# Optimization experiments

Hardware: AMD Instinct MI355X
Metric: run time of the kernel (lower is better)

Reference implementation:

```python
import jax, jax.numpy as jnp
import numpy as np

B_SZ, N_IN, N_CTX, UNITS, RANK = 4096, 4096, 512, 4096, 256


def setup_inputs() -> dict:
    key = jax.random.key(0)
    ks = jax.random.split(key, 8)
    inputs = jax.random.normal(ks[0], (B_SZ, N_IN), dtype=jnp.float32)
    context = jax.random.normal(ks[1], (B_SZ, N_CTX), dtype=jnp.float32)
    # Orthogonal-ish init approximated by scaled normals (math-equivalent shapes)
    U = jax.random.normal(ks[2], (N_IN, RANK), dtype=jnp.float32) / np.sqrt(N_IN)
    S = jax.random.uniform(ks[3], (RANK,), dtype=jnp.float32, minval=0.5, maxval=1.5)
    V = jax.random.normal(ks[4], (UNITS, RANK), dtype=jnp.float32) / np.sqrt(UNITS)
    W = jax.random.normal(ks[5], (N_CTX, RANK), dtype=jnp.float32) / np.sqrt(N_CTX)
    B = jnp.zeros((RANK,), dtype=jnp.float32)
    bias = jnp.zeros((UNITS,), dtype=jnp.float32)
    return {"inputs": inputs, "context": context, "U": U, "S": S, "V": V, "W": W, "B": B, "bias": bias}


def reference(inputs, context, U, S, V, W, B, bias):
    # chi[b,r] = sigmoid(context @ W + B)
    chi = jax.nn.sigmoid(context @ W + B)                  # [B, R]
    # Original: kernel[b,n,m] = sum_r U[n,r]*S[r]*chi[b,r]*V[m,r];
    # out[b,m] = sum_n x[b,n]*kernel[b,n,m]. Algebraically equal to:
    t = (inputs @ U) * (S * chi)                           # [B, R]
    out = t @ V.T + bias                                   # first '+ self.bias'
    out = out + bias                                       # 'outputs += self.bias' (use_bias=True)
    return jax.nn.relu(out)
```

## Files before the change

kernel.cpp:

```cpp
#include <hip/hip_runtime.h>

#define B_SZ 4096
#define N_IN 4096
#define N_CTX 512
#define UNITS 4096
#define RANK 256
#define ZSPLIT 8

typedef __attribute__((ext_vector_type(8))) __bf16 bf16x8;
typedef __attribute__((ext_vector_type(4))) float f32x4;
typedef __attribute__((ext_vector_type(8))) unsigned short ushort8;
typedef __attribute__((ext_vector_type(4))) unsigned short ushort4v;

__device__ __forceinline__ unsigned short f2bf(float f) {
    unsigned int u = __float_as_uint(f);
    u += 0x7FFFu + ((u >> 16) & 1u);
    return (unsigned short)(u >> 16);
}
__device__ __forceinline__ float bf2f(unsigned short h) {
    return __uint_as_float(((unsigned int)h) << 16);
}
__device__ __forceinline__ void gload_lds16(const unsigned short* g, unsigned short* l) {
    __builtin_amdgcn_global_load_lds(
        (const __attribute__((address_space(1))) unsigned int*)g,
        (__attribute__((address_space(3))) unsigned int*)l, 16, 0, 0);
}
__device__ __forceinline__ bf16x8 ldfrag(const unsigned short* p) {
    ushort8 t = *(const ushort8*)p;
    return __builtin_bit_cast(bf16x8, t);
}

__global__ void prep(const float* __restrict__ U, const float* __restrict__ W,
                     const float* __restrict__ V,
                     unsigned short* __restrict__ UT, unsigned short* __restrict__ WT,
                     unsigned short* __restrict__ Vb) {
    __shared__ unsigned short t[64][66];
    int bid = blockIdx.x, tid = threadIdx.x;
    if (bid < 288) {
        const float* src; unsigned short* dst; int R, C, rb, cb;
        if (bid < 256) { src = U; dst = UT; R = N_IN; C = RANK; rb = (bid & 63) * 64; cb = (bid >> 6) * 64; }
        else { int b = bid - 256; src = W; dst = WT; R = N_CTX; C = RANK; rb = (b & 7) * 64; cb = (b >> 3) * 64; }
        int r = tid >> 4, c4 = (tid & 15) * 4;
        for (int i = 0; i < 4; i++) {
            float4 v = *(const float4*)(src + (size_t)(rb + r + i * 16) * C + cb + c4);
            t[r + i * 16][c4 + 0] = f2bf(v.x);
            t[r + i * 16][c4 + 1] = f2bf(v.y);
            t[r + i * 16][c4 + 2] = f2bf(v.z);
            t[r + i * 16][c4 + 3] = f2bf(v.w);
        }
        __syncthreads();
        int c = tid >> 3, r8 = (tid & 7) * 8;
        for (int j = 0; j < 2; j++) {
            int cc = c + j * 32;
            ushort8 o;
            for (int k = 0; k < 8; k++) o[k] = t[r8 + k][cc];
            *(ushort8*)(dst + (size_t)(cb + cc) * R + rb + r8) = o;
        }
    } else {
        size_t base = (size_t)(bid - 288) * 2048 + (size_t)tid * 8;
        float4 a = *(const float4*)(V + base);
        float4 b = *(const float4*)(V + base + 4);
        ushort8 o = { f2bf(a.x), f2bf(a.y), f2bf(a.z), f2bf(a.w),
                      f2bf(b.x), f2bf(b.y), f2bf(b.z), f2bf(b.w) };
        *(ushort8*)(Vb + base) = o;
    }
}


__launch_bounds__(256, 4)
__global__ void k1_chi(const float* __restrict__ ctx, const unsigned short* __restrict__ WT,
                       const float* __restrict__ S, const float* __restrict__ Bb,
                       unsigned short* __restrict__ Schi) {
    __shared__ unsigned short As[32 * 64];
    __shared__ unsigned short Bs[64 * 64];
    int tid = threadIdx.x, w = tid >> 6, lane = tid & 63;
    int ln15 = lane & 15, quad = lane >> 4;
    int wr = w >> 1, wc = w & 1;
    int tm = blockIdx.y * 32, tn = blockIdx.x * 64;
    f32x4 acc2[2] = {};
    int arow = tid >> 3, acs = tid & 7;
    const float* ag = ctx + (size_t)(tm + arow) * N_CTX + acs * 8;
    unsigned short* al = As + arow * 64 + (acs ^ (arow & 7)) * 8;
    int bl8 = lane >> 3, bcs = lane & 7;
    int bgc = (bcs ^ bl8) * 8;
    for (int kt = 0; kt < 8; kt++) {
        int k0 = kt * 64;
        for (int c = 0; c < 2; c++) {
            int row = w * 16 + c * 8 + bl8;
            gload_lds16(WT + (size_t)(tn + row) * N_CTX + k0 + bgc, Bs + row * 64 + bcs * 8);
        }
        {
            float4 v0 = *(const float4*)(ag + k0);
            float4 v1 = *(const float4*)(ag + k0 + 4);
            ushort8 a8 = { f2bf(v0.x), f2bf(v0.y), f2bf(v0.z), f2bf(v0.w),
                           f2bf(v1.x), f2bf(v1.y), f2bf(v1.z), f2bf(v1.w) };
            *(ushort8*)al = a8;
        }
        __syncthreads();
        for (int kh = 0; kh < 2; kh++) {
            int ch = kh * 4 + quad;
            bf16x8 af = ldfrag(As + (wr * 16 + ln15) * 64 + (ch ^ (ln15 & 7)) * 8);
            for (int j = 0; j < 2; j++) {
                int row = wc * 32 + j * 16 + ln15;
                bf16x8 bfr = ldfrag(Bs + row * 64 + (ch ^ (ln15 & 7)) * 8);
                acc2[j] = __builtin_amdgcn_mfma_f32_16x16x32_bf16(af, bfr, acc2[j], 0, 0, 0);
            }
        }
        __syncthreads();
    }
    for (int j = 0; j < 2; j++) {
        int col = tn + wc * 32 + j * 16 + ln15;
        float sv = S[col], bv = Bb[col];
        for (int r = 0; r < 4; r++) {
            int row = tm + wr * 16 + quad * 4 + r;
            float x = acc2[j][r] + bv;
            float chi = sv / (1.f + __expf(-x));
            Schi[(size_t)row * RANK + col] = f2bf(chi);
        }
    }
}

__launch_bounds__(256, 4)
__global__ void k2_t0(const float* __restrict__ X, const unsigned short* __restrict__ UT,
                      unsigned short* __restrict__ T0p) {
    __shared__ unsigned short As[64 * 64];
    __shared__ unsigned short Bs[128 * 64];
    int tid = threadIdx.x, w = tid >> 6, lane = tid & 63;
    int ln15 = lane & 15, quad = lane >> 4;
    int wr = w >> 1, wc = w & 1;
    int tm = blockIdx.y * 64, tn = blockIdx.x * 128;
    int kbase = blockIdx.z * (N_IN / ZSPLIT);
    f32x4 acc[2][4] = {};
    int arow = tid >> 2, acs0 = tid & 3;
    const float* ag = X + (size_t)(tm + arow) * N_IN + kbase;
    unsigned short* al0 = As + arow * 64 + ((acs0 + 0) ^ (arow & 7)) * 8;
    unsigned short* al1 = As + arow * 64 + ((acs0 + 4) ^ (arow & 7)) * 8;
    int bl8 = lane >> 3, bcs = lane & 7;
    int bgc = (bcs ^ bl8) * 8;
    for (int kt = 0; kt < (N_IN / ZSPLIT) / 64; kt++) {
        int k0 = kt * 64;
        for (int c = 0; c < 4; c++) {
            int row = w * 32 + c * 8 + bl8;
            gload_lds16(UT + (size_t)(tn + row) * N_IN + kbase + k0 + bgc, Bs + row * 64 + bcs * 8);
        }
        {
            float4 v0 = *(const float4*)(ag + k0 + acs0 * 8);
            float4 v1 = *(const float4*)(ag + k0 + acs0 * 8 + 4);
            float4 u0 = *(const float4*)(ag + k0 + (acs0 + 4) * 8);
            float4 u1 = *(const float4*)(ag + k0 + (acs0 + 4) * 8 + 4);
            ushort8 a8 = { f2bf(v0.x), f2bf(v0.y), f2bf(v0.z), f2bf(v0.w),
                           f2bf(v1.x), f2bf(v1.y), f2bf(v1.z), f2bf(v1.w) };
            ushort8 b8 = { f2bf(u0.x), f2bf(u0.y), f2bf(u0.z), f2bf(u0.w),
                           f2bf(u1.x), f2bf(u1.y), f2bf(u1.z), f2bf(u1.w) };
            *(ushort8*)al0 = a8;
            *(ushort8*)al1 = b8;
        }
        __syncthreads();
        for (int kh = 0; kh < 2; kh++) {
            int ch = kh * 4 + quad;
            int sw = (ch ^ (ln15 & 7)) * 8;
            bf16x8 af[2], bfr[4];
            for (int i = 0; i < 2; i++)
                af[i] = ldfrag(As + (wr * 32 + i * 16 + ln15) * 64 + sw);
            for (int j = 0; j < 4; j++)
                bfr[j] = ldfrag(Bs + (wc * 64 + j * 16 + ln15) * 64 + sw);
            for (int i = 0; i < 2; i++)
                for (int j = 0; j < 4; j++)
                    acc[i][j] = __builtin_amdgcn_mfma_f32_16x16x32_bf16(af[i], bfr[j], acc[i][j], 0, 0, 0);
        }
        __syncthreads();
    }
    unsigned short* P = T0p + (size_t)blockIdx.z * B_SZ * RANK;
    for (int i = 0; i < 2; i++)
        for (int j = 0; j < 4; j++) {
            int col = tn + wc * 64 + j * 16 + ln15;
            for (int r = 0; r < 4; r++) {
                int row = tm + wr * 32 + i * 16 + quad * 4 + r;
                P[(size_t)row * RANK + col] = f2bf(acc[i][j][r]);
            }
        }
}

__global__ void e_red(const unsigned short* __restrict__ T0p, const unsigned short* __restrict__ Schi,
                      unsigned short* __restrict__ T) {
    int i = blockIdx.x * 256 + threadIdx.x;
    const size_t stride = (size_t)B_SZ * RANK;
    float a[8] = {};
    for (int z = 0; z < ZSPLIT; z++) {
        ushort8 p = *(const ushort8*)(T0p + z * stride + (size_t)i * 8);
        for (int k = 0; k < 8; k++) a[k] += bf2f(p[k]);
    }
    ushort8 s = *(const ushort8*)(Schi + (size_t)i * 8);
    ushort8 o;
    for (int k = 0; k < 8; k++) o[k] = f2bf(a[k] * bf2f(s[k]));
    *(ushort8*)(T + (size_t)i * 8) = o;
}

__launch_bounds__(256, 4)
__global__ void k3_out(const unsigned short* __restrict__ T, const unsigned short* __restrict__ Vb,
                       const float* __restrict__ bias, float* __restrict__ out) {
    __shared__ unsigned short As[64 * 64];
    __shared__ unsigned short Bs[128 * 64];
    int tid = threadIdx.x, w = tid >> 6, lane = tid & 63;
    int ln15 = lane & 15, quad = lane >> 4;
    int wr = w >> 1, wc = w & 1;
    int tn = blockIdx.x * 128, tm = blockIdx.y * 64;
    f32x4 acc[2][4] = {};
    int bl8 = lane >> 3, bcs = lane & 7;
    int bgc = (bcs ^ bl8) * 8;
    for (int kt = 0; kt < RANK / 64; kt++) {
        int k0 = kt * 64;
        for (int c = 0; c < 2; c++) {
            int row = w * 16 + c * 8 + bl8;
            gload_lds16(T + (size_t)(tm + row) * RANK + k0 + bgc, As + row * 64 + bcs * 8);
        }
        for (int c = 0; c < 4; c++) {
            int row = w * 32 + c * 8 + bl8;
            gload_lds16(Vb + (size_t)(tn + row) * RANK + k0 + bgc, Bs + row * 64 + bcs * 8);
        }
        __syncthreads();
        for (int kh = 0; kh < 2; kh++) {
            int ch = kh * 4 + quad;
            int sw = (ch ^ (ln15 & 7)) * 8;
            bf16x8 af[2], bfr[4];
            for (int i = 0; i < 2; i++)
                af[i] = ldfrag(As + (wr * 32 + i * 16 + ln15) * 64 + sw);
            for (int j = 0; j < 4; j++)
                bfr[j] = ldfrag(Bs + (wc * 64 + j * 16 + ln15) * 64 + sw);
            for (int i = 0; i < 2; i++)
                for (int j = 0; j < 4; j++)
                    acc[i][j] = __builtin_amdgcn_mfma_f32_16x16x32_bf16(af[i], bfr[j], acc[i][j], 0, 0, 0);
        }
        __syncthreads();
    }
    for (int j = 0; j < 4; j++) {
        int col = tn + wc * 64 + j * 16 + ln15;
        float bv = 2.f * bias[col];
        for (int i = 0; i < 2; i++)
            for (int r = 0; r < 4; r++) {
                int row = tm + wr * 32 + i * 16 + quad * 4 + r;
                float v = acc[i][j][r] + bv;
                out[(size_t)row * UNITS + col] = fmaxf(v, 0.f);
            }
    }
}

extern "C" void kernel_launch(void* const* d_in, const int* in_sizes, int n_in,
                              void* d_out, int out_size, void* d_ws, size_t ws_size,
                              hipStream_t stream) {
    (void)in_sizes; (void)n_in; (void)out_size; (void)ws_size;
    const float* inputs  = (const float*)d_in[0];
    const float* context = (const float*)d_in[1];
    const float* U       = (const float*)d_in[2];
    const float* S       = (const float*)d_in[3];
    const float* V       = (const float*)d_in[4];
    const float* W       = (const float*)d_in[5];
    const float* Bb      = (const float*)d_in[6];
    const float* bias    = (const float*)d_in[7];
    float* out = (float*)d_out;

    char* ws = (char*)d_ws;
    size_t o = 0;
    unsigned short* UT   = (unsigned short*)(ws + o); o += (size_t)RANK * N_IN * 2;
    unsigned short* WT   = (unsigned short*)(ws + o); o += (size_t)RANK * N_CTX * 2;
    unsigned short* Vb   = (unsigned short*)(ws + o); o += (size_t)UNITS * RANK * 2;
    unsigned short* Schi = (unsigned short*)(ws + o); o += (size_t)B_SZ * RANK * 2;
    unsigned short* T    = (unsigned short*)(ws + o); o += (size_t)B_SZ * RANK * 2;
    unsigned short* T0p  = (unsigned short*)(ws + o); o += (size_t)ZSPLIT * B_SZ * RANK * 2;

    prep<<<800, 256, 0, stream>>>(U, W, V, UT, WT, Vb);
    k2_t0<<<dim3(RANK / 128, B_SZ / 64, ZSPLIT), 256, 0, stream>>>(inputs, UT, T0p);
    k1_chi<<<dim3(RANK / 64, B_SZ / 32), 256, 0, stream>>>(context, WT, S, Bb, Schi);
    e_red<<<(B_SZ * RANK) / (256 * 8), 256, 0, stream>>>(T0p, Schi, T);
    k3_out<<<dim3(UNITS / 128, B_SZ / 64), 256, 0, stream>>>(T, Vb, bias, out);
}
```

Before: 178.8 us.

## Replace LDS-staged GEMM tiles with per-wave direct global fragment loads

```diff
diff --git a/kernel.cpp b/kernel.cpp
--- a/kernel.cpp
+++ b/kernel.cpp
@@ -10,7 +10,6 @@
 typedef __attribute__((ext_vector_type(8))) __bf16 bf16x8;
 typedef __attribute__((ext_vector_type(4))) float f32x4;
 typedef __attribute__((ext_vector_type(8))) unsigned short ushort8;
-typedef __attribute__((ext_vector_type(4))) unsigned short ushort4v;
 
 __device__ __forceinline__ unsigned short f2bf(float f) {
     unsigned int u = __float_as_uint(f);
@@ -20,15 +19,16 @@
 __device__ __forceinline__ float bf2f(unsigned short h) {
     return __uint_as_float(((unsigned int)h) << 16);
 }
-__device__ __forceinline__ void gload_lds16(const unsigned short* g, unsigned short* l) {
-    __builtin_amdgcn_global_load_lds(
-        (const __attribute__((address_space(1))) unsigned int*)g,
-        (__attribute__((address_space(3))) unsigned int*)l, 16, 0, 0);
-}
 __device__ __forceinline__ bf16x8 ldfrag(const unsigned short* p) {
     ushort8 t = *(const ushort8*)p;
     return __builtin_bit_cast(bf16x8, t);
 }
+__device__ __forceinline__ bf16x8 cvt8(float4 lo, float4 hi) {
+    ushort8 t = { f2bf(lo.x), f2bf(lo.y), f2bf(lo.z), f2bf(lo.w),
+                  f2bf(hi.x), f2bf(hi.y), f2bf(hi.z), f2bf(hi.w) };
+    return __builtin_bit_cast(bf16x8, t);
+}
+#define MFMA(a, b, c) __builtin_amdgcn_mfma_f32_16x16x32_bf16((a), (b), (c), 0, 0, 0)
 
 __global__ void prep(const float* __restrict__ U, const float* __restrict__ W,
                      const float* __restrict__ V,
@@ -66,116 +66,94 @@
     }
 }
 
-
-__launch_bounds__(256, 4)
+__launch_bounds__(128, 2)
 __global__ void k1_chi(const float* __restrict__ ctx, const unsigned short* __restrict__ WT,
                        const float* __restrict__ S, const float* __restrict__ Bb,
                        unsigned short* __restrict__ Schi) {
-    __shared__ unsigned short As[32 * 64];
-    __shared__ unsigned short Bs[64 * 64];
-    int tid = threadIdx.x, w = tid >> 6, lane = tid & 63;
+    int tid = threadIdx.x, wv = tid >> 6, lane = tid & 63;
     int ln15 = lane & 15, quad = lane >> 4;
-    int wr = w >> 1, wc = w & 1;
-    int tm = blockIdx.y * 32, tn = blockIdx.x * 64;
-    f32x4 acc2[2] = {};
-    int arow = tid >> 3, acs = tid & 7;
-    const float* ag = ctx + (size_t)(tm + arow) * N_CTX + acs * 8;
-    unsigned short* al = As + arow * 64 + (acs ^ (arow & 7)) * 8;
-    int bl8 = lane >> 3, bcs = lane & 7;
-    int bgc = (bcs ^ bl8) * 8;
-    for (int kt = 0; kt < 8; kt++) {
-        int k0 = kt * 64;
-        for (int c = 0; c < 2; c++) {
-            int row = w * 16 + c * 8 + bl8;
-            gload_lds16(WT + (size_t)(tn + row) * N_CTX + k0 + bgc, Bs + row * 64 + bcs * 8);
-        }
-        {
-            float4 v0 = *(const float4*)(ag + k0);
-            float4 v1 = *(const float4*)(ag + k0 + 4);
-            ushort8 a8 = { f2bf(v0.x), f2bf(v0.y), f2bf(v0.z), f2bf(v0.w),
-                           f2bf(v1.x), f2bf(v1.y), f2bf(v1.z), f2bf(v1.w) };
-            *(ushort8*)al = a8;
-        }
-        __syncthreads();
-        for (int kh = 0; kh < 2; kh++) {
-            int ch = kh * 4 + quad;
-            bf16x8 af = ldfrag(As + (wr * 16 + ln15) * 64 + (ch ^ (ln15 & 7)) * 8);
-            for (int j = 0; j < 2; j++) {
-                int row = wc * 32 + j * 16 + ln15;
-                bf16x8 bfr = ldfrag(Bs + row * 64 + (ch ^ (ln15 & 7)) * 8);
-                acc2[j] = __builtin_amdgcn_mfma_f32_16x16x32_bf16(af, bfr, acc2[j], 0, 0, 0);
-            }
-        }
-        __syncthreads();
-    }
-    for (int j = 0; j < 2; j++) {
-        int col = tn + wc * 32 + j * 16 + ln15;
+    int gw = blockIdx.x * 2 + wv;
+    int n0 = (gw & 3) * 64;
+    int m0 = (gw >> 2) * 16;
+    const float* Ap = ctx + (size_t)(m0 + ln15) * N_CTX + quad * 8;
+    const unsigned short* Bp = WT + (size_t)(n0 + ln15) * N_CTX + quad * 8;
+    f32x4 acc[4] = {};
+    for (int kt = 0; kt < N_CTX / 32; kt++) {
+        int ko = kt * 32;
+        float4 lo = *(const float4*)(Ap + ko);
+        float4 hi = *(const float4*)(Ap + ko + 4);
+        bf16x8 bfr[4];
+        #pragma unroll
+        for (int j = 0; j < 4; j++) bfr[j] = ldfrag(Bp + (size_t)j * 16 * N_CTX + ko);
+        bf16x8 af = cvt8(lo, hi);
+        #pragma unroll
+        for (int j = 0; j < 4; j++) acc[j] = MFMA(af, bfr[j], acc[j]);
+    }
+    #pragma unroll
+    for (int j = 0; j < 4; j++) {
+        int col = n0 + j * 16 + ln15;
         float sv = S[col], bv = Bb[col];
+        #pragma unroll
         for (int r = 0; r < 4; r++) {
-            int row = tm + wr * 16 + quad * 4 + r;
-            float x = acc2[j][r] + bv;
-            float chi = sv / (1.f + __expf(-x));
-            Schi[(size_t)row * RANK + col] = f2bf(chi);
-        }
-    }
-}
-
-__launch_bounds__(256, 4)
+            int row = m0 + quad * 4 + r;
+            float x = acc[j][r] + bv;
+            Schi[(size_t)row * RANK + col] = f2bf(sv / (1.f + __expf(-x)));
+        }
+    }
+}
+
+__launch_bounds__(128, 2)
 __global__ void k2_t0(const float* __restrict__ X, const unsigned short* __restrict__ UT,
                       unsigned short* __restrict__ T0p) {
-    __shared__ unsigned short As[64 * 64];
-    __shared__ unsigned short Bs[128 * 64];
-    int tid = threadIdx.x, w = tid >> 6, lane = tid & 63;
+    int tid = threadIdx.x, wv = tid >> 6, lane = tid & 63;
     int ln15 = lane & 15, quad = lane >> 4;
-    int wr = w >> 1, wc = w & 1;
-    int tm = blockIdx.y * 64, tn = blockIdx.x * 128;
-    int kbase = blockIdx.z * (N_IN / ZSPLIT);
-    f32x4 acc[2][4] = {};
-    int arow = tid >> 2, acs0 = tid & 3;
-    const float* ag = X + (size_t)(tm + arow) * N_IN + kbase;
-    unsigned short* al0 = As + arow * 64 + ((acs0 + 0) ^ (arow & 7)) * 8;
-    unsigned short* al1 = As + arow * 64 + ((acs0 + 4) ^ (arow & 7)) * 8;
-    int bl8 = lane >> 3, bcs = lane & 7;
-    int bgc = (bcs ^ bl8) * 8;
-    for (int kt = 0; kt < (N_IN / ZSPLIT) / 64; kt++) {
-        int k0 = kt * 64;
-        for (int c = 0; c < 4; c++) {
-            int row = w * 32 + c * 8 + bl8;
-            gload_lds16(UT + (size_t)(tn + row) * N_IN + kbase + k0 + bgc, Bs + row * 64 + bcs * 8);
-        }
-        {
-            float4 v0 = *(const float4*)(ag + k0 + acs0 * 8);
-            float4 v1 = *(const float4*)(ag + k0 + acs0 * 8 + 4);
-            float4 u0 = *(const float4*)(ag + k0 + (acs0 + 4) * 8);
-            float4 u1 = *(const float4*)(ag + k0 + (acs0 + 4) * 8 + 4);
-            ushort8 a8 = { f2bf(v0.x), f2bf(v0.y), f2bf(v0.z), f2bf(v0.w),
-                           f2bf(v1.x), f2bf(v1.y), f2bf(v1.z), f2bf(v1.w) };
-            ushort8 b8 = { f2bf(u0.x), f2bf(u0.y), f2bf(u0.z), f2bf(u0.w),
-                           f2bf(u1.x), f2bf(u1.y), f2bf(u1.z), f2bf(u1.w) };
-            *(ushort8*)al0 = a8;
-            *(ushort8*)al1 = b8;
-        }
-        __syncthreads();
-        for (int kh = 0; kh < 2; kh++) {
-            int ch = kh * 4 + quad;
-            int sw = (ch ^ (ln15 & 7)) * 8;
-            bf16x8 af[2], bfr[4];
-            for (int i = 0; i < 2; i++)
-                af[i] = ldfrag(As + (wr * 32 + i * 16 + ln15) * 64 + sw);
-            for (int j = 0; j < 4; j++)
-                bfr[j] = ldfrag(Bs + (wc * 64 + j * 16 + ln15) * 64 + sw);
-            for (int i = 0; i < 2; i++)
-                for (int j = 0; j < 4; j++)
-                    acc[i][j] = __builtin_amdgcn_mfma_f32_16x16x32_bf16(af[i], bfr[j], acc[i][j], 0, 0, 0);
-        }
-        __syncthreads();
-    }
-    unsigned short* P = T0p + (size_t)blockIdx.z * B_SZ * RANK;
+    int gw = blockIdx.x * 2 + wv;
+    int z = gw >> 8;
+    int m0 = ((gw >> 1) & 127) * 32;
+    int n0 = (gw & 1) * 128;
+    const int kbase = z * (N_IN / ZSPLIT);
+
+    const float* Xp  = X + (size_t)(m0 + ln15) * N_IN + kbase + quad * 8;
+    const float* Xp2 = Xp + (size_t)16 * N_IN;
+    const unsigned short* Bp = UT + (size_t)(n0 + ln15) * N_IN + kbase + quad * 8;
+
+    f32x4 acc[2][8] = {};
+    float4 a[2][2][2];
+    a[0][0][0] = *(const float4*)(Xp);
+    a[0][0][1] = *(const float4*)(Xp + 4);
+    a[0][1][0] = *(const float4*)(Xp2);
+    a[0][1][1] = *(const float4*)(Xp2 + 4);
+
+    for (int kt = 0; kt < 16; kt++) {
+        int cur = kt & 1, nxt = cur ^ 1;
+        if (kt < 15) {
+            int ko = (kt + 1) * 32;
+            a[nxt][0][0] = *(const float4*)(Xp + ko);
+            a[nxt][0][1] = *(const float4*)(Xp + ko + 4);
+            a[nxt][1][0] = *(const float4*)(Xp2 + ko);
+            a[nxt][1][1] = *(const float4*)(Xp2 + ko + 4);
+        }
+        bf16x8 bfr[8];
+        #pragma unroll
+        for (int j = 0; j < 8; j++)
+            bfr[j] = ldfrag(Bp + (size_t)j * 16 * N_IN + kt * 32);
+        bf16x8 af0 = cvt8(a[cur][0][0], a[cur][0][1]);
+        bf16x8 af1 = cvt8(a[cur][1][0], a[cur][1][1]);
+        #pragma unroll
+        for (int j = 0; j < 8; j++) {
+            acc[0][j] = MFMA(af0, bfr[j], acc[0][j]);
+            acc[1][j] = MFMA(af1, bfr[j], acc[1][j]);
+        }
+    }
+    unsigned short* P = T0p + (size_t)z * B_SZ * RANK;
+    #pragma unroll
     for (int i = 0; i < 2; i++)
-        for (int j = 0; j < 4; j++) {
-            int col = tn + wc * 64 + j * 16 + ln15;
+        #pragma unroll
+        for (int j = 0; j < 8; j++) {
+            int col = n0 + j * 16 + ln15;
+            #pragma unroll
             for (int r = 0; r < 4; r++) {
-                int row = tm + wr * 32 + i * 16 + quad * 4 + r;
+                int row = m0 + i * 16 + quad * 4 + r;
                 P[(size_t)row * RANK + col] = f2bf(acc[i][j][r]);
             }
         }
@@ -196,49 +174,40 @@
     *(ushort8*)(T + (size_t)i * 8) = o;
 }
 
-__launch_bounds__(256, 4)
+__launch_bounds__(256, 3)
 __global__ void k3_out(const unsigned short* __restrict__ T, const unsigned short* __restrict__ Vb,
                        const float* __restrict__ bias, float* __restrict__ out) {
-    __shared__ unsigned short As[64 * 64];
-    __shared__ unsigned short Bs[128 * 64];
-    int tid = threadIdx.x, w = tid >> 6, lane = tid & 63;
+    int tid = threadIdx.x, wv = tid >> 6, lane = tid & 63;
     int ln15 = lane & 15, quad = lane >> 4;
-    int wr = w >> 1, wc = w & 1;
-    int tn = blockIdx.x * 128, tm = blockIdx.y * 64;
-    f32x4 acc[2][4] = {};
-    int bl8 = lane >> 3, bcs = lane & 7;
-    int bgc = (bcs ^ bl8) * 8;
-    for (int kt = 0; kt < RANK / 64; kt++) {
-        int k0 = kt * 64;
-        for (int c = 0; c < 2; c++) {
-            int row = w * 16 + c * 8 + bl8;
-            gload_lds16(T + (size_t)(tm + row) * RANK + k0 + bgc, As + row * 64 + bcs * 8);
-        }
-        for (int c = 0; c < 4; c++) {
-            int row = w * 32 + c * 8 + bl8;
-            gload_lds16(Vb + (size_t)(tn + row) * RANK + k0 + bgc, Bs + row * 64 + bcs * 8);
-        }
-        __syncthreads();
-        for (int kh = 0; kh < 2; kh++) {
-            int ch = kh * 4 + quad;
-            int sw = (ch ^ (ln15 & 7)) * 8;
-            bf16x8 af[2], bfr[4];
-            for (int i = 0; i < 2; i++)
-                af[i] = ldfrag(As + (wr * 32 + i * 16 + ln15) * 64 + sw);
-            for (int j = 0; j < 4; j++)
-                bfr[j] = ldfrag(Bs + (wc * 64 + j * 16 + ln15) * 64 + sw);
-            for (int i = 0; i < 2; i++)
-                for (int j = 0; j < 4; j++)
-                    acc[i][j] = __builtin_amdgcn_mfma_f32_16x16x32_bf16(af[i], bfr[j], acc[i][j], 0, 0, 0);
-        }
-        __syncthreads();
-    }
-    for (int j = 0; j < 4; j++) {
-        int col = tn + wc * 64 + j * 16 + ln15;
+    int gw = blockIdx.x * 4 + wv;
+    int n0 = (gw & 31) * 128;
+    int m0 = (gw >> 5) * 32;
+    const unsigned short* Ap  = T + (size_t)(m0 + ln15) * RANK + quad * 8;
+    const unsigned short* Ap2 = Ap + (size_t)16 * RANK;
+    const unsigned short* Bp  = Vb + (size_t)(n0 + ln15) * RANK + quad * 8;
+    f32x4 acc[2][8] = {};
+    for (int kt = 0; kt < RANK / 32; kt++) {
+        int ko = kt * 32;
+        bf16x8 af0 = ldfrag(Ap + ko);
+        bf16x8 af1 = ldfrag(Ap2 + ko);
+        bf16x8 bfr[8];
+        #pragma unroll
+        for (int j = 0; j < 8; j++) bfr[j] = ldfrag(Bp + (size_t)j * 16 * RANK + ko);
+        #pragma unroll
+        for (int j = 0; j < 8; j++) {
+            acc[0][j] = MFMA(af0, bfr[j], acc[0][j]);
+            acc[1][j] = MFMA(af1, bfr[j], acc[1][j]);
+        }
+    }
+    #pragma unroll
+    for (int j = 0; j < 8; j++) {
+        int col = n0 + j * 16 + ln15;
         float bv = 2.f * bias[col];
+        #pragma unroll
         for (int i = 0; i < 2; i++)
+            #pragma unroll
             for (int r = 0; r < 4; r++) {
-                int row = tm + wr * 32 + i * 16 + quad * 4 + r;
+                int row = m0 + i * 16 + quad * 4 + r;
                 float v = acc[i][j][r] + bv;
                 out[(size_t)row * UNITS + col] = fmaxf(v, 0.f);
             }
@@ -269,8 +238,8 @@
     unsigned short* T0p  = (unsigned short*)(ws + o); o += (size_t)ZSPLIT * B_SZ * RANK * 2;
 
     prep<<<800, 256, 0, stream>>>(U, W, V, UT, WT, Vb);
-    k2_t0<<<dim3(RANK / 128, B_SZ / 64, ZSPLIT), 256, 0, stream>>>(inputs, UT, T0p);
-    k1_chi<<<dim3(RANK / 64, B_SZ / 32), 256, 0, stream>>>(context, WT, S, Bb, Schi);
+    k2_t0<<<1024, 128, 0, stream>>>(inputs, UT, T0p);
+    k1_chi<<<512, 128, 0, stream>>>(context, WT, S, Bb, Schi);
     e_red<<<(B_SZ * RANK) / (256 * 8), 256, 0, stream>>>(T0p, Schi, T);
-    k3_out<<<dim3(UNITS / 128, B_SZ / 64), 256, 0, stream>>>(T, Vb, bias, out);
-}
+    k3_out<<<1024, 256, 0, stream>>>(T, Vb, bias, out);
+}
```

Measured after the change: 231.3 us. 1.29x slower.
